# Performance work log

Measured on AMD Instinct MI355X. Metric: run time of the kernel, lower is better.

## Reference

```python
import jax, jax.numpy as jnp
import numpy as np

N_NODES = 100000
N_EDGES = 1250000
N_GRAPHS = 256
IN_DIM, HID, OUT = 7, 64, 2


def setup_inputs() -> dict:
    key = jax.random.key(0)
    ks = jax.random.split(key, 10)
    x = jax.random.normal(ks[0], (N_NODES, IN_DIM), dtype=jnp.float32)
    edge_index = jax.random.randint(ks[1], (2, N_EDGES), 0, N_NODES, dtype=jnp.int64)
    batch = jnp.sort(jax.random.randint(ks[2], (N_NODES,), 0, N_GRAPHS, dtype=jnp.int64))
    def glorot(k, shape):
        lim = float(np.sqrt(6.0 / (shape[0] + shape[1])))
        return jax.random.uniform(k, shape, jnp.float32, -lim, lim)
    return {
        "x": x, "edge_index": edge_index, "batch": batch,
        "W1": glorot(ks[3], (IN_DIM, HID)), "b1": jnp.zeros((HID,), jnp.float32),
        "W2": glorot(ks[4], (HID, HID)),   "b2": jnp.zeros((HID,), jnp.float32),
        "W3": glorot(ks[5], (HID, HID)),   "b3": jnp.zeros((HID,), jnp.float32),
        "Wl": glorot(ks[6], (HID, OUT)),   "bl": jnp.zeros((OUT,), jnp.float32),
    }


def _gcn_conv(x, src, dst, W, b, n_nodes):
    # PyG GCNConv: add self-loops, symmetric deg^{-1/2} normalization,
    # linear transform, scatter-add aggregation at target nodes, + bias.
    deg = jax.ops.segment_sum(jnp.ones_like(dst, dtype=x.dtype), dst, num_segments=n_nodes)
    dinv = jnp.where(deg > 0, jax.lax.rsqrt(deg), 0.0)
    norm = dinv[src] * dinv[dst]                      # [E+N]
    h = x @ W                                         # [N, out]
    msg = h[src] * norm[:, None]                      # gather + scale
    out = jax.ops.segment_sum(msg, dst, num_segments=n_nodes)
    return out + b


def reference(x, edge_index, batch, W1, b1, W2, b2, W3, b3, Wl, bl):
    n = x.shape[0]
    loop = jnp.arange(n, dtype=edge_index.dtype)
    src = jnp.concatenate([edge_index[0], loop])      # self-loops appended once
    dst = jnp.concatenate([edge_index[1], loop])

    h = jax.nn.relu(_gcn_conv(x, src, dst, W1, b1, n))
    h = jax.nn.relu(_gcn_conv(h, src, dst, W2, b2, n))
    h = _gcn_conv(h, src, dst, W3, b3, n)

    # global_mean_pool over graphs
    sums = jax.ops.segment_sum(h, batch, num_segments=N_GRAPHS)
    cnt = jax.ops.segment_sum(jnp.ones((n,), h.dtype), batch, num_segments=N_GRAPHS)
    pooled = sums / jnp.maximum(cnt, 1.0)[:, None]    # [G, HID]

    # dropout is identity in eval mode
    return pooled @ Wl + bl                           # [G, 2]
```

## Files before the change

### kernel.cpp

```cpp
#include <hip/hip_runtime.h>
#include <hip/hip_fp16.h>

#define HID 64
#define NGRAPHS 256
#define CHUNK 4096
#define BKTSZ 512
#define BKTSH 9
#define PSH 17
#define PMASK 0x1FFFF

typedef _Float16 half8 __attribute__((ext_vector_type(8)));
typedef float f32x4 __attribute__((ext_vector_type(4)));



__global__ __launch_bounds__(256) void k_hist(
        const int* __restrict__ dst, const float* __restrict__ W2,
        const float* __restrict__ W3, __half* __restrict__ Wf2,
        __half* __restrict__ Wf3, int* __restrict__ H,
        float* __restrict__ gsum, int e, int nbkt, int nchunk) {
    __shared__ int cnt4[4][256];
    const int t = threadIdx.x, b = blockIdx.x;
    const int gtid = b * 256 + t;
    if (gtid < 512) {
        int p = gtid;
        int kt = p >> 8, c = (p >> 6) & 3, lane = p & 63;
        int quad = lane >> 4, m = lane & 15;
#pragma unroll
        for (int j = 0; j < 8; ++j) {
            int k = kt * 32 + quad * 8 + j;
            int ch = c * 16 + m;
            Wf2[(size_t)p * 8 + j] = __float2half(W2[k * HID + ch]);
            Wf3[(size_t)p * 8 + j] = __float2half(W3[k * HID + ch]);
        }
    }
    if (b == 0) {
        for (int i = t; i < NGRAPHS * HID; i += 256) gsum[i] = 0.0f;
    }
    for (int i = t; i < 1024; i += 256) ((int*)cnt4)[i] = 0;
    __syncthreads();
    const int w = t >> 6;
#pragma unroll
    for (int it = 0; it < CHUNK / 1024; ++it) {
        int idx = b * CHUNK + it * 1024 + t * 4;
        if (idx + 3 < e) {
            int4 d = *(const int4*)(dst + idx);
            atomicAdd(&cnt4[w][d.x >> BKTSH], 1);
            atomicAdd(&cnt4[w][d.y >> BKTSH], 1);
            atomicAdd(&cnt4[w][d.z >> BKTSH], 1);
            atomicAdd(&cnt4[w][d.w >> BKTSH], 1);
        } else {
            for (int i = idx; i < e && i < idx + 4; ++i)
                atomicAdd(&cnt4[w][dst[i] >> BKTSH], 1);
        }
    }
    __syncthreads();
    for (int i = t; i < nbkt; i += 256)
        H[i * nchunk + b] = cnt4[0][i] + cnt4[1][i] + cnt4[2][i] + cnt4[3][i];
}


__global__ __launch_bounds__(256) void k_scan(const int* __restrict__ in,
                                              int* __restrict__ outp,
                                              int* __restrict__ bsum, int n) {
    __shared__ int sh[256];
    const int t = threadIdx.x;
    const int base = blockIdx.x * 1024 + t * 4;
    int v[4];
    int s = 0;
#pragma unroll
    for (int k = 0; k < 4; k++) {
        int i = base + k;
        v[k] = (i < n) ? in[i] : 0;
        s += v[k];
    }
    sh[t] = s;
    __syncthreads();
#pragma unroll
    for (int off = 1; off < 256; off <<= 1) {
        int add = (t >= off) ? sh[t - off] : 0;
        __syncthreads();
        sh[t] += add;
        __syncthreads();
    }
    int run = sh[t] - s;
#pragma unroll
    for (int k = 0; k < 4; k++) {
        int i = base + k;
        if (i < n) outp[i] = run;
        run += v[k];
    }
    if (t == 255) bsum[blockIdx.x] = sh[255];
}


__global__ __launch_bounds__(256) void k_scatter(
        const int* __restrict__ src, const int* __restrict__ dst,
        const int* __restrict__ Hs, const int* __restrict__ bsum,
        int* __restrict__ packed, int e, int nbkt, int nchunk, int nscan) {
    __shared__ int off[256];
    __shared__ int lc[256];
    __shared__ int bscan[64];
    const int t = threadIdx.x, b = blockIdx.x;
    if (t < 64) bscan[t] = (t < nscan) ? bsum[t] : 0;
    __syncthreads();
#pragma unroll
    for (int o = 1; o < 64; o <<= 1) {
        int add = (t < 64 && t >= o) ? bscan[t - o] : 0;
        __syncthreads();
        if (t < 64) bscan[t] += add;
        __syncthreads();
    }
    for (int i = t; i < nbkt; i += 256) {
        int idx = i * nchunk + b;
        int q = idx >> 10;
        off[i] = Hs[idx] + (q ? bscan[q - 1] : 0);
        lc[i] = 0;
    }
    __syncthreads();
#pragma unroll
    for (int it = 0; it < CHUNK / 1024; ++it) {
        int idx = b * CHUNK + it * 1024 + t * 4;
        if (idx + 3 < e) {
            int4 d = *(const int4*)(dst + idx);
            int4 s = *(const int4*)(src + idx);
            int b0 = d.x >> BKTSH, b1 = d.y >> BKTSH;
            int b2 = d.z >> BKTSH, b3 = d.w >> BKTSH;
            int r0 = atomicAdd(&lc[b0], 1);
            int r1 = atomicAdd(&lc[b1], 1);
            int r2 = atomicAdd(&lc[b2], 1);
            int r3 = atomicAdd(&lc[b3], 1);
            packed[off[b0] + r0] = s.x | ((d.x & (BKTSZ - 1)) << PSH);
            packed[off[b1] + r1] = s.y | ((d.y & (BKTSZ - 1)) << PSH);
            packed[off[b2] + r2] = s.z | ((d.z & (BKTSZ - 1)) << PSH);
            packed[off[b3] + r3] = s.w | ((d.w & (BKTSZ - 1)) << PSH);
        } else {
            for (int i = idx; i < e && i < idx + 4; ++i) {
                int dd = dst[i];
                int bk = dd >> BKTSH;
                int r = atomicAdd(&lc[bk], 1);
                packed[off[bk] + r] = src[i] | ((dd & (BKTSZ - 1)) << PSH);
            }
        }
    }
}


__global__ __launch_bounds__(256) void k_csr_build(
        const int* __restrict__ packed, const int* __restrict__ Hs,
        const int* __restrict__ bsum, int* __restrict__ rowptr,
        float* __restrict__ dinv, int* __restrict__ csr,
        int e, int n, int nbkt, int nchunk, int nscan) {
    __shared__ int cnt[BKTSZ];
    __shared__ int pref[BKTSZ];
    __shared__ int ssum[256];
    __shared__ int cnt2[BKTSZ];
    __shared__ int bscan[64];
    const int t = threadIdx.x, bkt = blockIdx.x;
    if (t < 64) bscan[t] = (t < nscan) ? bsum[t] : 0;
    if (bkt == 0 && t == 0) rowptr[n] = e;
    cnt[t] = 0; cnt[t + 256] = 0;
    cnt2[t] = 0; cnt2[t + 256] = 0;
    __syncthreads();
#pragma unroll
    for (int o = 1; o < 64; o <<= 1) {
        int add = (t < 64 && t >= o) ? bscan[t - o] : 0;
        __syncthreads();
        if (t < 64) bscan[t] += add;
        __syncthreads();
    }
    int i0 = bkt * nchunk;
    int q0 = i0 >> 10;
    int segStart = Hs[i0] + (q0 ? bscan[q0 - 1] : 0);
    int segEnd = e;
    if (bkt + 1 < nbkt) {
        int i1 = (bkt + 1) * nchunk;
        int q1 = i1 >> 10;
        segEnd = Hs[i1] + (q1 ? bscan[q1 - 1] : 0);
    }
    for (int j = segStart + t; j < segEnd; j += 256)
        atomicAdd(&cnt[(packed[j] >> PSH) & (BKTSZ - 1)], 1);
    __syncthreads();
    int a0 = cnt[2 * t], a1 = cnt[2 * t + 1];
    int s = a0 + a1;
    ssum[t] = s;
    __syncthreads();
#pragma unroll
    for (int off = 1; off < 256; off <<= 1) {
        int add = (t >= off) ? ssum[t - off] : 0;
        __syncthreads();
        ssum[t] += add;
        __syncthreads();
    }
    int p = ssum[t] - s;
    pref[2 * t] = p;
    pref[2 * t + 1] = p + a0;
    __syncthreads();
    for (int i = t; i < BKTSZ; i += 256) {
        int node = bkt * BKTSZ + i;
        if (node < n) {
            rowptr[node] = segStart + pref[i];
            dinv[node] = rsqrtf((float)(cnt[i] + 1));
        }
    }
    for (int j = segStart + t; j < segEnd; j += 256) {
        int pk = packed[j];
        int ld = (pk >> PSH) & (BKTSZ - 1);
        int r = atomicAdd(&cnt2[ld], 1);
        csr[segStart + pref[ld] + r] = pk & PMASK;
    }
}


__global__ __launch_bounds__(256) void k_gemm7(
        const float* __restrict__ act, const float* __restrict__ W,
        const float* __restrict__ dinv, __half* __restrict__ h, int n_nodes) {
    __shared__ float Wsh[7 * HID];
    __shared__ float Ash[16 * 7];
    const int t = threadIdx.x;
    const int n0 = blockIdx.x * 16;

    for (int i = t; i < 7 * HID; i += 256) Wsh[i] = W[i];
    const long long lim = (long long)(n_nodes - n0) * 7;
    for (int i = t; i < 16 * 7; i += 256)
        Ash[i] = (i < lim) ? act[(size_t)n0 * 7 + i] : 0.0f;
    __syncthreads();

    const int c = t & 63;
    const int g = t >> 6;
    float acc[4] = {0.0f, 0.0f, 0.0f, 0.0f};
#pragma unroll
    for (int k = 0; k < 7; k++) {
        float w = Wsh[k * HID + c];
#pragma unroll
        for (int i = 0; i < 4; i++) acc[i] += Ash[(g * 4 + i) * 7 + k] * w;
    }
#pragma unroll
    for (int i = 0; i < 4; i++) {
        int n = n0 + g * 4 + i;
        if (n < n_nodes) h[(size_t)n * HID + c] = __float2half(acc[i] * dinv[n]);
    }
}

__device__ __forceinline__ float4 h4_to_f4(int2 raw) {
    __half2 p0 = *(__half2*)&raw.x;
    __half2 p1 = *(__half2*)&raw.y;
    float2 f0 = __half22float2(p0);
    float2 f1 = __half22float2(p1);
    return make_float4(f0.x, f0.y, f1.x, f1.y);
}


__global__ __launch_bounds__(256) void k_agg_gemm(
        const int* __restrict__ rowptr, const int* __restrict__ csr,
        const __half* __restrict__ h, const float* __restrict__ b,
        const float* __restrict__ dinv, const __half* __restrict__ Wf,
        __half* __restrict__ hout, int n_nodes) {
    __shared__ __half act[16 * 72];
    const int t = threadIdx.x;
    const int n0 = blockIdx.x * 16;
    const int nl = t >> 4;
    const int node = n0 + nl;
    const int l16 = t & 15;
    const int2* h8 = (const int2*)h;
    const float4* b4 = (const float4*)b;

    float4 av = make_float4(0.0f, 0.0f, 0.0f, 0.0f);
    if (node < n_nodes) {
        int beg = rowptr[node], end = rowptr[node + 1];
        float dv = dinv[node];
        float4 inner = h4_to_f4(h8[(size_t)node * 16 + l16]);
        int j = beg;
        for (; j + 7 < end; j += 8) {
            int s[8];
#pragma unroll
            for (int q = 0; q < 8; ++q) s[q] = csr[j + q];
            int2 r[8];
#pragma unroll
            for (int q = 0; q < 8; ++q) r[q] = h8[(size_t)s[q] * 16 + l16];
#pragma unroll
            for (int q = 0; q < 8; ++q) {
                float4 v = h4_to_f4(r[q]);
                inner.x += v.x; inner.y += v.y; inner.z += v.z; inner.w += v.w;
            }
        }
        for (; j + 3 < end; j += 4) {
            int s0 = csr[j], s1 = csr[j + 1], s2 = csr[j + 2], s3 = csr[j + 3];
            float4 v0 = h4_to_f4(h8[(size_t)s0 * 16 + l16]);
            float4 v1 = h4_to_f4(h8[(size_t)s1 * 16 + l16]);
            float4 v2 = h4_to_f4(h8[(size_t)s2 * 16 + l16]);
            float4 v3 = h4_to_f4(h8[(size_t)s3 * 16 + l16]);
            inner.x += v0.x + v1.x + v2.x + v3.x;
            inner.y += v0.y + v1.y + v2.y + v3.y;
            inner.z += v0.z + v1.z + v2.z + v3.z;
            inner.w += v0.w + v1.w + v2.w + v3.w;
        }
        for (; j < end; j++) {
            float4 v = h4_to_f4(h8[(size_t)csr[j] * 16 + l16]);
            inner.x += v.x; inner.y += v.y; inner.z += v.z; inner.w += v.w;
        }
        float4 bb = b4[l16];
        av.x = fmaxf(bb.x + dv * inner.x, 0.0f);
        av.y = fmaxf(bb.y + dv * inner.y, 0.0f);
        av.z = fmaxf(bb.z + dv * inner.z, 0.0f);
        av.w = fmaxf(bb.w + dv * inner.w, 0.0f);
    }
    {
        __half2 p0 = __floats2half2_rn(av.x, av.y);
        __half2 p1 = __floats2half2_rn(av.z, av.w);
        int2 pk;
        pk.x = *(int*)&p0;
        pk.y = *(int*)&p1;
        *(int2*)&act[nl * 72 + l16 * 4] = pk;
    }
    __syncthreads();

    const int wave = t >> 6, lane = t & 63;
    const int quad = lane >> 4, m = lane & 15;
    const half8* Wf8 = (const half8*)Wf;
    f32x4 acc = {0.0f, 0.0f, 0.0f, 0.0f};
#pragma unroll
    for (int kt = 0; kt < 2; ++kt) {
        half8 a = *(const half8*)&act[m * 72 + kt * 32 + quad * 8];
        half8 bv = Wf8[(kt * 4 + wave) * 64 + lane];
        acc = __builtin_amdgcn_mfma_f32_16x16x32_f16(a, bv, acc, 0, 0, 0);
    }
#pragma unroll
    for (int r = 0; r < 4; ++r) {
        int nd = n0 + quad * 4 + r;
        if (nd < n_nodes)
            hout[(size_t)nd * HID + wave * 16 + m] =
                __float2half(acc[r] * dinv[nd]);
    }
}


__global__ __launch_bounds__(256) void k_agg_part(
        const int* __restrict__ rowptr, const int* __restrict__ csr,
        const __half* __restrict__ h, const float* __restrict__ b,
        const float* __restrict__ dinv, const int* __restrict__ batch,
        float* __restrict__ partv, int* __restrict__ partg,
        float* __restrict__ gsum, int n_nodes) {
    __shared__ float redbuf[16][64];
    __shared__ int bg[16];
    const int t = threadIdx.x;
    const int n0 = blockIdx.x * 16;
    const int nl = t >> 4;
    const int node = n0 + nl;
    const int l16 = t & 15;
    const int2* h8 = (const int2*)h;
    const float4* b4 = (const float4*)b;

    if (t < 16) {
        int nd = n0 + t;
        bg[t] = (nd < n_nodes) ? batch[nd] : -1;
    }

    float4 res = make_float4(0.0f, 0.0f, 0.0f, 0.0f);
    if (node < n_nodes) {
        int beg = rowptr[node], end = rowptr[node + 1];
        float dv = dinv[node];
        float4 inner = h4_to_f4(h8[(size_t)node * 16 + l16]);
        int j = beg;
        for (; j + 7 < end; j += 8) {
            int s[8];
#pragma unroll
            for (int q = 0; q < 8; ++q) s[q] = csr[j + q];
            int2 r[8];
#pragma unroll
            for (int q = 0; q < 8; ++q) r[q] = h8[(size_t)s[q] * 16 + l16];
#pragma unroll
            for (int q = 0; q < 8; ++q) {
                float4 v = h4_to_f4(r[q]);
                inner.x += v.x; inner.y += v.y; inner.z += v.z; inner.w += v.w;
            }
        }
        for (; j + 3 < end; j += 4) {
            int s0 = csr[j], s1 = csr[j + 1], s2 = csr[j + 2], s3 = csr[j + 3];
            float4 v0 = h4_to_f4(h8[(size_t)s0 * 16 + l16]);
            float4 v1 = h4_to_f4(h8[(size_t)s1 * 16 + l16]);
            float4 v2 = h4_to_f4(h8[(size_t)s2 * 16 + l16]);
            float4 v3 = h4_to_f4(h8[(size_t)s3 * 16 + l16]);
            inner.x += v0.x + v1.x + v2.x + v3.x;
            inner.y += v0.y + v1.y + v2.y + v3.y;
            inner.z += v0.z + v1.z + v2.z + v3.z;
            inner.w += v0.w + v1.w + v2.w + v3.w;
        }
        for (; j < end; j++) {
            float4 v = h4_to_f4(h8[(size_t)csr[j] * 16 + l16]);
            inner.x += v.x; inner.y += v.y; inner.z += v.z; inner.w += v.w;
        }
        float4 bb = b4[l16];
        res.x = bb.x + dv * inner.x;
        res.y = bb.y + dv * inner.y;
        res.z = bb.z + dv * inner.z;
        res.w = bb.w + dv * inner.w;
    }
    *(float4*)&redbuf[nl][l16 * 4] = res;
    __syncthreads();

    if (t < 64) {
        const int c = t;
        const int g0 = bg[0];
        const int g15 = bg[15];
        float s0 = 0.0f, s1 = 0.0f;
        for (int i = 0; i < 16; ++i) {
            int g = bg[i];
            float v = redbuf[i][c];
            if (g == g0) s0 += v;
            else if (g == g15) s1 += v;
            else if (g >= 0) atomicAdd(&gsum[g * HID + c], v);
        }
        partv[(size_t)blockIdx.x * 128 + c] = s0;
        partv[(size_t)blockIdx.x * 128 + 64 + c] = s1;
        if (c == 0) {
            partg[blockIdx.x * 2 + 0] = g0;
            partg[blockIdx.x * 2 + 1] = (g15 != g0) ? g15 : -1;
        }
    }
}


__global__ __launch_bounds__(256) void k_pool_head(
        const float* __restrict__ partv, const int* __restrict__ partg,
        const float* __restrict__ gsum, const int* __restrict__ batch,
        const float* __restrict__ Wl, const float* __restrict__ bl,
        float* __restrict__ out, int n_nodes) {
    int g = blockIdx.x;
    int lo = 0, hi = n_nodes;
    while (lo < hi) { int m = (lo + hi) >> 1; if (batch[m] < g) lo = m + 1; else hi = m; }
    int nstart = lo;
    hi = n_nodes;
    while (lo < hi) { int m = (lo + hi) >> 1; if (batch[m] < g + 1) lo = m + 1; else hi = m; }
    int nend = lo;

    int c = threadIdx.x & 63, part = threadIdx.x >> 6;
    float acc = 0.0f;
    if (nend > nstart) {
        int b0 = nstart >> 4, b1 = (nend - 1) >> 4;
        for (int b = b0 + part; b <= b1; b += 4) {
            if (partg[b * 2 + 0] == g) acc += partv[(size_t)b * 128 + c];
            if (partg[b * 2 + 1] == g) acc += partv[(size_t)b * 128 + 64 + c];
        }
    }

    __shared__ float red[4][64];
    __shared__ float hd[128];
    red[part][c] = acc;
    __syncthreads();
    if (threadIdx.x < 64) {
        float cntf = (float)(nend - nstart);
        float pooled = (red[0][c] + red[1][c] + red[2][c] + red[3][c]
                        + gsum[g * HID + c]) / fmaxf(cntf, 1.0f);
        hd[c] = pooled * Wl[c * 2 + 0];
        hd[64 + c] = pooled * Wl[c * 2 + 1];
    }
    __syncthreads();
    if (threadIdx.x < 2) {
        float s = 0.0f;
        for (int k = 0; k < 64; k++) s += hd[threadIdx.x * 64 + k];
        out[g * 2 + threadIdx.x] = s + bl[threadIdx.x];
    }
}


extern "C" void kernel_launch(void* const* d_in, const int* in_sizes, int n_in,
                              void* d_out, int out_size, void* d_ws, size_t ws_size,
                              hipStream_t stream) {
    const float* x     = (const float*)d_in[0];
    const int*   ei    = (const int*)d_in[1];
    const int*   batch = (const int*)d_in[2];
    const float* W1    = (const float*)d_in[3];
    const float* b1    = (const float*)d_in[4];
    const float* W2    = (const float*)d_in[5];
    const float* b2    = (const float*)d_in[6];
    const float* W3    = (const float*)d_in[7];
    const float* b3    = (const float*)d_in[8];
    const float* Wl    = (const float*)d_in[9];
    const float* bl    = (const float*)d_in[10];
    float* out = (float*)d_out;

    const int N = in_sizes[0] / 7;
    const int E = in_sizes[1] / 2;
    const int* src = ei;
    const int* dst = ei + E;

    const int nbkt   = (N + BKTSZ - 1) >> BKTSH;
    const int nchunk = (E + CHUNK - 1) / CHUNK;
    const int lenH   = nbkt * nchunk;
    const int nscan  = (lenH + 1023) / 1024;

    char* ws = (char*)d_ws;
    size_t off = 0;
    auto carve = [&](size_t bytes) {
        void* p = ws + off;
        off = (off + bytes + 255) & ~(size_t)255;
        return p;
    };
    int*    H      = (int*)carve((size_t)lenH * 4);
    int*    Hs     = (int*)carve((size_t)lenH * 4);
    int*    bsum   = (int*)carve(512 * 4);
    int*    packed = (int*)carve((size_t)E * 4);
    int*    csr    = (int*)carve((size_t)E * 4);
    int*    rowptr = (int*)carve((size_t)(N + 1) * 4);
    float*  dinv   = (float*)carve((size_t)N * 4);
    __half* Wf2    = (__half*)carve(4096 * 2);
    __half* Wf3    = (__half*)carve(4096 * 2);
    float*  gsum   = (float*)carve((size_t)NGRAPHS * HID * 4);
    __half* bufH   = (__half*)carve((size_t)(N + 64) * HID * 2);
    __half* bufB   = (__half*)carve((size_t)(N + 64) * HID * 2);

    const int nb_gemm7 = (N + 15) / 16;
    const int nb_agg   = (N + 15) / 16;
    float* partv = (float*)carve((size_t)nb_agg * 128 * 4);
    int*   partg = (int*)carve((size_t)nb_agg * 2 * 4);

    k_hist<<<nchunk, 256, 0, stream>>>(dst, W2, W3, Wf2, Wf3, H, gsum,
                                       E, nbkt, nchunk);
    k_scan<<<nscan, 256, 0, stream>>>(H, Hs, bsum, lenH);
    k_scatter<<<nchunk, 256, 0, stream>>>(src, dst, Hs, bsum, packed,
                                          E, nbkt, nchunk, nscan);
    k_csr_build<<<nbkt, 256, 0, stream>>>(packed, Hs, bsum, rowptr, dinv, csr,
                                          E, N, nbkt, nchunk, nscan);

    k_gemm7<<<nb_gemm7, 256, 0, stream>>>(x, W1, dinv, bufH, N);
    k_agg_gemm<<<nb_agg, 256, 0, stream>>>(rowptr, csr, bufH, b1, dinv, Wf2, bufB, N);
    k_agg_gemm<<<nb_agg, 256, 0, stream>>>(rowptr, csr, bufB, b2, dinv, Wf3, bufH, N);
    k_agg_part<<<nb_agg, 256, 0, stream>>>(rowptr, csr, bufH, b3, dinv, batch,
                                           partv, partg, gsum, N);

    k_pool_head<<<NGRAPHS, 256, 0, stream>>>(partv, partg, gsum, batch,
                                             Wl, bl, out, N);
}
```

Measured before the change: 236.0 us.

## Fuse first-layer GEMM into CSR build and shuffle-broadcast edge indices

The 7->64 first-layer transform is folded into the CSR-build kernel, reusing the per-bucket degree counts already in shared memory to compute dinv. This removes a separate kernel launch and its dinv reload. The aggregation loops now load 8 (or 4) CSR indices cooperatively, one per lane, and broadcast them with __shfl instead of every lane loading all indices. The fused kernel gains about 16KB of shared memory, which may lower its occupancy, and its 4-wide remainder block now runs at most once before the scalar tail.

```diff
diff --git a/kernel.cpp b/kernel.cpp
--- a/kernel.cpp
+++ b/kernel.cpp
@@ -150,15 +150,26 @@
         const int* __restrict__ packed, const int* __restrict__ Hs,
         const int* __restrict__ bsum, int* __restrict__ rowptr,
         float* __restrict__ dinv, int* __restrict__ csr,
+        const float* __restrict__ x, const float* __restrict__ W1,
+        __half* __restrict__ h1,
         int e, int n, int nbkt, int nchunk, int nscan) {
     __shared__ int cnt[BKTSZ];
     __shared__ int pref[BKTSZ];
     __shared__ int ssum[256];
     __shared__ int cnt2[BKTSZ];
     __shared__ int bscan[64];
+    __shared__ float Wsh[7 * HID];
+    __shared__ float Xsh[BKTSZ * 7];
     const int t = threadIdx.x, bkt = blockIdx.x;
     if (t < 64) bscan[t] = (t < nscan) ? bsum[t] : 0;
     if (bkt == 0 && t == 0) rowptr[n] = e;
+    for (int i = t; i < 7 * HID; i += 256) Wsh[i] = W1[i];
+    {
+        const int xbase = bkt * BKTSZ * 7;
+        const int xlim = n * 7 - xbase;
+        for (int i = t; i < BKTSZ * 7; i += 256)
+            Xsh[i] = (i < xlim) ? x[xbase + i] : 0.0f;
+    }
     cnt[t] = 0; cnt[t + 256] = 0;
     cnt2[t] = 0; cnt2[t + 256] = 0;
     __syncthreads();
@@ -209,36 +220,18 @@
         int r = atomicAdd(&cnt2[ld], 1);
         csr[segStart + pref[ld] + r] = pk & PMASK;
     }
-}
-
-
-__global__ __launch_bounds__(256) void k_gemm7(
-        const float* __restrict__ act, const float* __restrict__ W,
-        const float* __restrict__ dinv, __half* __restrict__ h, int n_nodes) {
-    __shared__ float Wsh[7 * HID];
-    __shared__ float Ash[16 * 7];
-    const int t = threadIdx.x;
-    const int n0 = blockIdx.x * 16;
-
-    for (int i = t; i < 7 * HID; i += 256) Wsh[i] = W[i];
-    const long long lim = (long long)(n_nodes - n0) * 7;
-    for (int i = t; i < 16 * 7; i += 256)
-        Ash[i] = (i < lim) ? act[(size_t)n0 * 7 + i] : 0.0f;
-    __syncthreads();
-
     const int c = t & 63;
     const int g = t >> 6;
-    float acc[4] = {0.0f, 0.0f, 0.0f, 0.0f};
-#pragma unroll
-    for (int k = 0; k < 7; k++) {
-        float w = Wsh[k * HID + c];
-#pragma unroll
-        for (int i = 0; i < 4; i++) acc[i] += Ash[(g * 4 + i) * 7 + k] * w;
-    }
-#pragma unroll
-    for (int i = 0; i < 4; i++) {
-        int n = n0 + g * 4 + i;
-        if (n < n_nodes) h[(size_t)n * HID + c] = __float2half(acc[i] * dinv[n]);
+    for (int it2 = 0; it2 < BKTSZ / 4; ++it2) {
+        int nl = it2 * 4 + g;
+        int node = bkt * BKTSZ + nl;
+        if (node >= n) break;
+        float acc = 0.0f;
+#pragma unroll
+        for (int k = 0; k < 7; ++k)
+            acc += Xsh[nl * 7 + k] * Wsh[k * HID + c];
+        float dv = rsqrtf((float)(cnt[nl] + 1));
+        h1[(size_t)node * HID + c] = __float2half(acc * dv);
     }
 }
 
@@ -272,28 +265,29 @@
         float4 inner = h4_to_f4(h8[(size_t)node * 16 + l16]);
         int j = beg;
         for (; j + 7 < end; j += 8) {
-            int s[8];
-#pragma unroll
-            for (int q = 0; q < 8; ++q) s[q] = csr[j + q];
+            int e8 = csr[j + (l16 & 7)];
             int2 r[8];
 #pragma unroll
-            for (int q = 0; q < 8; ++q) r[q] = h8[(size_t)s[q] * 16 + l16];
+            for (int q = 0; q < 8; ++q)
+                r[q] = h8[(size_t)__shfl(e8, q, 8) * 16 + l16];
 #pragma unroll
             for (int q = 0; q < 8; ++q) {
                 float4 v = h4_to_f4(r[q]);
                 inner.x += v.x; inner.y += v.y; inner.z += v.z; inner.w += v.w;
             }
         }
-        for (; j + 3 < end; j += 4) {
-            int s0 = csr[j], s1 = csr[j + 1], s2 = csr[j + 2], s3 = csr[j + 3];
-            float4 v0 = h4_to_f4(h8[(size_t)s0 * 16 + l16]);
-            float4 v1 = h4_to_f4(h8[(size_t)s1 * 16 + l16]);
-            float4 v2 = h4_to_f4(h8[(size_t)s2 * 16 + l16]);
-            float4 v3 = h4_to_f4(h8[(size_t)s3 * 16 + l16]);
-            inner.x += v0.x + v1.x + v2.x + v3.x;
-            inner.y += v0.y + v1.y + v2.y + v3.y;
-            inner.z += v0.z + v1.z + v2.z + v3.z;
-            inner.w += v0.w + v1.w + v2.w + v3.w;
+        if (j + 3 < end) {
+            int e4 = csr[j + (l16 & 3)];
+            int2 r[4];
+#pragma unroll
+            for (int q = 0; q < 4; ++q)
+                r[q] = h8[(size_t)__shfl(e4, q, 4) * 16 + l16];
+#pragma unroll
+            for (int q = 0; q < 4; ++q) {
+                float4 v = h4_to_f4(r[q]);
+                inner.x += v.x; inner.y += v.y; inner.z += v.z; inner.w += v.w;
+            }
+            j += 4;
         }
         for (; j < end; j++) {
             float4 v = h4_to_f4(h8[(size_t)csr[j] * 16 + l16]);
@@ -363,28 +357,29 @@
         float4 inner = h4_to_f4(h8[(size_t)node * 16 + l16]);
         int j = beg;
         for (; j + 7 < end; j += 8) {
-            int s[8];
-#pragma unroll
-            for (int q = 0; q < 8; ++q) s[q] = csr[j + q];
+            int e8 = csr[j + (l16 & 7)];
             int2 r[8];
 #pragma unroll
-            for (int q = 0; q < 8; ++q) r[q] = h8[(size_t)s[q] * 16 + l16];
+            for (int q = 0; q < 8; ++q)
+                r[q] = h8[(size_t)__shfl(e8, q, 8) * 16 + l16];
 #pragma unroll
             for (int q = 0; q < 8; ++q) {
                 float4 v = h4_to_f4(r[q]);
                 inner.x += v.x; inner.y += v.y; inner.z += v.z; inner.w += v.w;
             }
         }
-        for (; j + 3 < end; j += 4) {
-            int s0 = csr[j], s1 = csr[j + 1], s2 = csr[j + 2], s3 = csr[j + 3];
-            float4 v0 = h4_to_f4(h8[(size_t)s0 * 16 + l16]);
-            float4 v1 = h4_to_f4(h8[(size_t)s1 * 16 + l16]);
-            float4 v2 = h4_to_f4(h8[(size_t)s2 * 16 + l16]);
-            float4 v3 = h4_to_f4(h8[(size_t)s3 * 16 + l16]);
-            inner.x += v0.x + v1.x + v2.x + v3.x;
-            inner.y += v0.y + v1.y + v2.y + v3.y;
-            inner.z += v0.z + v1.z + v2.z + v3.z;
-            inner.w += v0.w + v1.w + v2.w + v3.w;
+        if (j + 3 < end) {
+            int e4 = csr[j + (l16 & 3)];
+            int2 r[4];
+#pragma unroll
+            for (int q = 0; q < 4; ++q)
+                r[q] = h8[(size_t)__shfl(e4, q, 4) * 16 + l16];
+#pragma unroll
+            for (int q = 0; q < 4; ++q) {
+                float4 v = h4_to_f4(r[q]);
+                inner.x += v.x; inner.y += v.y; inner.z += v.z; inner.w += v.w;
+            }
+            j += 4;
         }
         for (; j < end; j++) {
             float4 v = h4_to_f4(h8[(size_t)csr[j] * 16 + l16]);
@@ -510,8 +505,7 @@
     __half* bufH   = (__half*)carve((size_t)(N + 64) * HID * 2);
     __half* bufB   = (__half*)carve((size_t)(N + 64) * HID * 2);
 
-    const int nb_gemm7 = (N + 15) / 16;
-    const int nb_agg   = (N + 15) / 16;
+    const int nb_agg = (N + 15) / 16;
     float* partv = (float*)carve((size_t)nb_agg * 128 * 4);
     int*   partg = (int*)carve((size_t)nb_agg * 2 * 4);
 
@@ -521,9 +515,9 @@
     k_scatter<<<nchunk, 256, 0, stream>>>(src, dst, Hs, bsum, packed,
                                           E, nbkt, nchunk, nscan);
     k_csr_build<<<nbkt, 256, 0, stream>>>(packed, Hs, bsum, rowptr, dinv, csr,
+                                          x, W1, bufH,
                                           E, N, nbkt, nchunk, nscan);
 
-    k_gemm7<<<nb_gemm7, 256, 0, stream>>>(x, W1, dinv, bufH, N);
     k_agg_gemm<<<nb_agg, 256, 0, stream>>>(rowptr, csr, bufH, b1, dinv, Wf2, bufB, N);
     k_agg_gemm<<<nb_agg, 256, 0, stream>>>(rowptr, csr, bufB, b2, dinv, Wf3, bufH, N);
     k_agg_part<<<nb_agg, 256, 0, stream>>>(rowptr, csr, bufH, b3, dinv, batch,
```

New measurement: 248.4 us. 1.05x slower.
